# Performance work log

Hardware: AMD Instinct MI355X
Metric: run time of the kernel (lower is better)

The kernel has to match this reference:

```python
import jax, jax.numpy as jnp
import numpy as np

N = 100000
E = 1000000
IN_DIM = 128
HID = 32
HEADS = 4
OUT_DIM = 64
NEG_SLOPE = 0.2


def _gat_layer(x, src, dst, W, a_src, a_dst, b, heads, out_ch, concat):
    n = x.shape[0]
    h = (x @ W).reshape(n, heads, out_ch)                     # [N,H,C]
    s_src = jnp.sum(h * a_src, axis=-1)                        # [N,H]
    s_dst = jnp.sum(h * a_dst, axis=-1)                        # [N,H]
    e = jax.nn.leaky_relu(s_src[src] + s_dst[dst], NEG_SLOPE)  # [E,H]
    # segment softmax over incoming edges of each destination node
    m = jax.ops.segment_max(e, dst, num_segments=n)            # [N,H]
    w = jnp.exp(e - m[dst])                                    # [E,H]
    denom = jax.ops.segment_sum(w, dst, num_segments=n)        # [N,H]
    alpha = w / denom[dst]                                     # [E,H]
    out = jax.ops.segment_sum(h[src] * alpha[:, :, None], dst, num_segments=n)  # [N,H,C]
    out = out.reshape(n, heads * out_ch) if concat else out[:, 0, :]
    return out + b


def setup_inputs() -> dict:
    key = jax.random.key(0)
    ks = jax.random.split(key, 12)
    g = 0.1
    return {
        "x": jax.random.normal(ks[0], (N, IN_DIM), dtype=jnp.float32),
        "edge_index": jax.random.randint(ks[1], (2, E), 0, N, dtype=jnp.int64),
        "W1": jax.random.normal(ks[2], (IN_DIM, HEADS * HID), dtype=jnp.float32) * g,
        "a_src1": jax.random.normal(ks[3], (HEADS, HID), dtype=jnp.float32) * g,
        "a_dst1": jax.random.normal(ks[4], (HEADS, HID), dtype=jnp.float32) * g,
        "b1": jnp.zeros((HEADS * HID,), dtype=jnp.float32),
        "W2": jax.random.normal(ks[5], (HEADS * HID, OUT_DIM), dtype=jnp.float32) * g,
        "a_src2": jax.random.normal(ks[6], (1, OUT_DIM), dtype=jnp.float32) * g,
        "a_dst2": jax.random.normal(ks[7], (1, OUT_DIM), dtype=jnp.float32) * g,
        "b2": jnp.zeros((OUT_DIM,), dtype=jnp.float32),
        "fc_W": jax.random.normal(ks[8], (OUT_DIM, OUT_DIM), dtype=jnp.float32) * g,
        "fc_b": jnp.zeros((OUT_DIM,), dtype=jnp.float32),
    }


def reference(x, edge_index, W1, a_src1, a_dst1, b1, W2, a_src2, a_dst2, b2, fc_W, fc_b):
    # PyG GATConv adds self-loops by default
    loop = jnp.arange(N, dtype=edge_index.dtype)
    src = jnp.concatenate([edge_index[0], loop])
    dst = jnp.concatenate([edge_index[1], loop])
    h = _gat_layer(x, src, dst, W1, a_src1, a_dst1, b1, HEADS, HID, concat=True)
    h = jax.nn.relu(h)
    h = _gat_layer(h, src, dst, W2, a_src2, a_dst2, b2, 1, OUT_DIM, concat=False)
    h = h @ fc_W + fc_b
    return jax.nn.log_softmax(h, axis=1)
```

## Files before the change

kernel.cpp:

```cpp
#include <hip/hip_runtime.h>
#include <hip/hip_bf16.h>
#include <cfloat>

#define NN 100000
#define EE 1000000
#define TE (EE + NN)
#define C1 128
#define C2 64
#define NB1 782
#define NBKT 782
#define BCAP 4096

typedef unsigned short u16;
typedef unsigned int u32;
using bf16x8 = __attribute__((ext_vector_type(8))) short;
using f32x4  = __attribute__((ext_vector_type(4))) float;

__device__ __forceinline__ float lrelu(float v) { return v > 0.f ? v : 0.2f * v; }
__device__ __forceinline__ u16 f2bf(float f) {
    u32 b = __float_as_uint(f);
    b += 0x7fffu + ((b >> 16) & 1u);
    return (u16)(b >> 16);
}
__device__ __forceinline__ float bflo(u32 p) { return __uint_as_float(p << 16); }
__device__ __forceinline__ float bfhi(u32 p) { return __uint_as_float(p & 0xffff0000u); }

__global__ __launch_bounds__(64) void kprep(const float* __restrict__ W2,
    const float* __restrict__ as2, const float* __restrict__ ad2,
    const float* __restrict__ b2, const float* __restrict__ fcW,
    const float* __restrict__ fcb, const float* __restrict__ W1,
    u16* __restrict__ W2pbt, u16* __restrict__ W1bt,
    float* __restrict__ us, float* __restrict__ ud, float* __restrict__ b2p) {
    int b = blockIdx.x, t = threadIdx.x;
    if (b < 128) {
        float s = 0.f;
        for (int k = 0; k < 64; ++k) s = fmaf(W2[b * 64 + k], fcW[k * 64 + t], s);
        W2pbt[t * 128 + b] = f2bf(s);
    } else if (b < 130) {
        int r = (b - 128) * 64 + t;
        float s = 0.f, d = 0.f;
        for (int k = 0; k < 64; ++k) {
            float wv = W2[r * 64 + k];
            s = fmaf(wv, as2[k], s);
            d = fmaf(wv, ad2[k], d);
        }
        us[r] = s; ud[r] = d;
    } else if (b == 130) {
        float s = fcb[t];
        for (int k = 0; k < 64; ++k) s = fmaf(b2[k], fcW[k * 64 + t], s);
        b2p[t] = s;
    } else {
        int c = b - 131;
        W1bt[c * 128 + t]      = f2bf(W1[t * 128 + c]);
        W1bt[c * 128 + 64 + t] = f2bf(W1[(64 + t) * 128 + c]);
    }
}

__global__ __launch_bounds__(256) void kpassA(const int* __restrict__ esrc,
    const int* __restrict__ edst, int* __restrict__ bcnt, u32* __restrict__ bbuf) {
    int i = blockIdx.x * 256 + threadIdx.x;
    if (i >= EE / 4) return;
    int4 s4 = ((const int4*)esrc)[i];
    int4 d4 = ((const int4*)edst)[i];
    int d, s, b, pos;
    d = d4.x; s = s4.x; b = d >> 7;
    pos = atomicAdd(bcnt + b * 16, 1);
    if (pos < BCAP) bbuf[(size_t)b * BCAP + pos] = (u32)s | ((u32)(d & 127) << 17);
    d = d4.y; s = s4.y; b = d >> 7;
    pos = atomicAdd(bcnt + b * 16, 1);
    if (pos < BCAP) bbuf[(size_t)b * BCAP + pos] = (u32)s | ((u32)(d & 127) << 17);
    d = d4.z; s = s4.z; b = d >> 7;
    pos = atomicAdd(bcnt + b * 16, 1);
    if (pos < BCAP) bbuf[(size_t)b * BCAP + pos] = (u32)s | ((u32)(d & 127) << 17);
    d = d4.w; s = s4.w; b = d >> 7;
    pos = atomicAdd(bcnt + b * 16, 1);
    if (pos < BCAP) bbuf[(size_t)b * BCAP + pos] = (u32)s | ((u32)(d & 127) << 17);
}

__global__ __launch_bounds__(1024) void kbscan(const int* __restrict__ bcnt,
                                               int* __restrict__ bbase) {
    __shared__ int sm[1024];
    int t = threadIdx.x;
    int v = 0;
    if (t < NBKT) {
        int node0 = t * 128;
        int nn = NN - node0; if (nn > 128) nn = 128;
        int m = bcnt[t * 16]; if (m > BCAP) m = BCAP;
        v = m + nn;
    }
    sm[t] = v;
    __syncthreads();
    for (int off = 1; off < 1024; off <<= 1) {
        int o = 0;
        if (t >= off) o = sm[t - off];
        __syncthreads();
        if (t >= off) sm[t] += o;
        __syncthreads();
    }
    if (t < NBKT) bbase[t] = sm[t] - v;
}

__global__ __launch_bounds__(256) void kpassB(const int* __restrict__ bcnt,
    const int* __restrict__ bbase, const u32* __restrict__ bbuf,
    int* __restrict__ rowstart, int* __restrict__ eidx) {
    __shared__ int deg[128], lsc[128], cur[128];
    __shared__ int elocal[BCAP + 128];
    int b = blockIdx.x, t = threadIdx.x;
    int node0 = b * 128;
    int nNodes = NN - node0; if (nNodes > 128) nNodes = 128;
    int M = bcnt[b * 16]; if (M > BCAP) M = BCAP;
    int base = bbase[b];
    if (t < 128) deg[t] = 0;
    __syncthreads();
    const u32* bp = bbuf + (size_t)b * BCAP;
    for (int i = t; i < M; i += 256) atomicAdd(&deg[bp[i] >> 17], 1);
    __syncthreads();
    int v = 0;
    if (t < 128) { v = (t < nNodes) ? (1 + deg[t]) : 0; lsc[t] = v; }
    __syncthreads();
    for (int off = 1; off < 128; off <<= 1) {
        int o = 0;
        if (t < 128 && t >= off) o = lsc[t - off];
        __syncthreads();
        if (t < 128 && t >= off) lsc[t] += o;
        __syncthreads();
    }
    if (t < nNodes) {
        int st = lsc[t] - v;
        rowstart[node0 + t] = base + st;
        elocal[st] = node0 + t;
        cur[t] = st + 1;
    }
    if (b == NBKT - 1 && t == 0) rowstart[NN] = TE;
    __syncthreads();
    for (int i = t; i < M; i += 256) {
        u32 p = bp[i];
        int pos = atomicAdd(&cur[p >> 17], 1);
        elocal[pos] = (int)(p & 0x1FFFFu);
    }
    __syncthreads();
    int total = M + nNodes;
    for (int i = t; i < total; i += 256) eidx[base + i] = elocal[i];
}

__global__ __launch_bounds__(256, 1) void k1_mfma(const float* __restrict__ x,
    const u16* __restrict__ W1bt, const float* __restrict__ as1,
    const float* __restrict__ ad1, u16* __restrict__ h1b,
    float* __restrict__ ssrc, float* __restrict__ sdst) {
    __shared__ u16 As[128][136];
    __shared__ u16 Bs[128][136];
    int t = threadIdx.x;
    int rbase = blockIdx.x * 128;
    #pragma unroll
    for (int j = 0; j < 8; ++j) {
        int i = t + 256 * j, row = i >> 4, seg = i & 15;
        *reinterpret_cast<uint4*>(&Bs[row][seg * 8]) =
            *reinterpret_cast<const uint4*>(W1bt + row * 128 + seg * 8);
    }
    #pragma unroll
    for (int j = 0; j < 16; ++j) {
        int i = t + 256 * j, row = i >> 5, c4 = i & 31;
        int gr = rbase + row; if (gr >= NN) gr = NN - 1;
        float4 v = *reinterpret_cast<const float4*>(x + (size_t)gr * 128 + c4 * 4);
        ushort4 o2 = make_ushort4(f2bf(v.x), f2bf(v.y), f2bf(v.z), f2bf(v.w));
        *reinterpret_cast<ushort4*>(&As[row][c4 * 4]) = o2;
    }
    __syncthreads();
    int lane = t & 63, wv = t >> 6, wr = wv >> 1, wc = wv & 1;
    int fr = lane & 15, fg = lane >> 4;
    f32x4 acc[4][4];
    #pragma unroll
    for (int m = 0; m < 4; ++m)
        #pragma unroll
        for (int n = 0; n < 4; ++n) acc[m][n] = (f32x4){0.f, 0.f, 0.f, 0.f};
    #pragma unroll
    for (int kk = 0; kk < 4; ++kk) {
        bf16x8 af[4], bfr[4];
        #pragma unroll
        for (int m = 0; m < 4; ++m)
            af[m] = *reinterpret_cast<const bf16x8*>(&As[wr * 64 + m * 16 + fr][kk * 32 + fg * 8]);
        #pragma unroll
        for (int n = 0; n < 4; ++n)
            bfr[n] = *reinterpret_cast<const bf16x8*>(&Bs[wc * 64 + n * 16 + fr][kk * 32 + fg * 8]);
        #pragma unroll
        for (int m = 0; m < 4; ++m)
            #pragma unroll
            for (int n = 0; n < 4; ++n)
                acc[m][n] = __builtin_amdgcn_mfma_f32_16x16x32_bf16(af[m], bfr[n], acc[m][n], 0, 0, 0);
    }
    float asv[4], adv[4];
    #pragma unroll
    for (int n = 0; n < 4; ++n) {
        int col = wc * 64 + n * 16 + fr;
        asv[n] = as1[col]; adv[n] = ad1[col];
    }
    #pragma unroll
    for (int m = 0; m < 4; ++m)
        #pragma unroll
        for (int r = 0; r < 4; ++r) {
            int row = rbase + wr * 64 + m * 16 + fg * 4 + r;
            bool ok = row < NN;
            if (ok) {
                #pragma unroll
                for (int n = 0; n < 4; ++n)
                    h1b[(size_t)row * 128 + wc * 64 + n * 16 + fr] = f2bf(acc[m][n][r]);
            }
            float psA = acc[m][0][r] * asv[0] + acc[m][1][r] * asv[1];
            float psB = acc[m][2][r] * asv[2] + acc[m][3][r] * asv[3];
            float pdA = acc[m][0][r] * adv[0] + acc[m][1][r] * adv[1];
            float pdB = acc[m][2][r] * adv[2] + acc[m][3][r] * adv[3];
            #pragma unroll
            for (int off = 1; off <= 8; off <<= 1) {
                psA += __shfl_xor(psA, off); psB += __shfl_xor(psB, off);
                pdA += __shfl_xor(pdA, off); pdB += __shfl_xor(pdB, off);
            }
            if (fr == 0 && ok) {
                ssrc[row * 4 + 2 * wc]     = psA; sdst[row * 4 + 2 * wc]     = pdA;
                ssrc[row * 4 + 2 * wc + 1] = psB; sdst[row * 4 + 2 * wc + 1] = pdB;
            }
        }
}

__global__ __launch_bounds__(256) void agg1(const int* __restrict__ rowstart,
    const int* __restrict__ eidx, const float* __restrict__ ssrc,
    const float* __restrict__ sdst, const u16* __restrict__ h1b,
    const float* __restrict__ b1, const float* __restrict__ usv,
    const float* __restrict__ udv, u16* __restrict__ hrb,
    float* __restrict__ ssrc2, float* __restrict__ sdst2) {
    int lane = threadIdx.x & 63;
    int n = blockIdx.x * 4 + (threadIdx.x >> 6);
    if (n >= NN) return;
    int r0 = rowstart[n], deg = rowstart[n + 1] - r0;
    int h4 = lane >> 4, j16 = lane & 15;
    int half = lane >> 5, c = lane & 31, hh = c >> 3;
    float sd = sdst[n * 4 + h4];
    int s0 = (j16 < deg) ? eidx[r0 + j16] : eidx[r0];
    uint2 pv[8];
    #pragma unroll
    for (int q = 0; q < 8; ++q) {
        int s = __shfl(s0, 2 * q + half);
        pv[q] = *(const uint2*)(h1b + (size_t)s * C1 + 4 * c);
    }
    float sv0 = (j16 < deg) ? lrelu(ssrc[s0 * 4 + h4] + sd) : -FLT_MAX;
    float mx = sv0;
    #pragma unroll
    for (int off = 1; off <= 8; off <<= 1) mx = fmaxf(mx, __shfl_xor(mx, off));
    for (int base = 16; base < deg; base += 16) {
        int j = base + j16;
        float sv = (j < deg) ? lrelu(ssrc[eidx[r0 + j] * 4 + h4] + sd) : -FLT_MAX;
        #pragma unroll
        for (int off = 1; off <= 8; off <<= 1) sv = fmaxf(sv, __shfl_xor(sv, off));
        mx = fmaxf(mx, sv);
    }
    float w = (j16 < deg) ? __expf(sv0 - mx) : 0.f;
    float den = w;
    float a0 = 0.f, a1 = 0.f, a2 = 0.f, a3 = 0.f;
    #pragma unroll
    for (int q = 0; q < 8; ++q) {
        float wq = __shfl(w, (hh << 4) + 2 * q + half);
        a0 = fmaf(wq, bflo(pv[q].x), a0);
        a1 = fmaf(wq, bfhi(pv[q].x), a1);
        a2 = fmaf(wq, bflo(pv[q].y), a2);
        a3 = fmaf(wq, bfhi(pv[q].y), a3);
    }
    for (int base = 16; base < deg; base += 16) {
        int j = base + j16;
        int sreg = (j < deg) ? eidx[r0 + j] : eidx[r0];
        uint2 qv[8];
        #pragma unroll
        for (int q = 0; q < 8; ++q) {
            int s = __shfl(sreg, 2 * q + half);
            qv[q] = *(const uint2*)(h1b + (size_t)s * C1 + 4 * c);
        }
        float wb = (j < deg) ? __expf(lrelu(ssrc[sreg * 4 + h4] + sd) - mx) : 0.f;
        den += wb;
        #pragma unroll
        for (int q = 0; q < 8; ++q) {
            float wq = __shfl(wb, (hh << 4) + 2 * q + half);
            a0 = fmaf(wq, bflo(qv[q].x), a0);
            a1 = fmaf(wq, bfhi(qv[q].x), a1);
            a2 = fmaf(wq, bflo(qv[q].y), a2);
            a3 = fmaf(wq, bfhi(qv[q].y), a3);
        }
    }
    #pragma unroll
    for (int off = 1; off <= 8; off <<= 1) den += __shfl_xor(den, off);
    float dh = __shfl(den, hh << 4);
    a0 += __shfl_xor(a0, 32);
    a1 += __shfl_xor(a1, 32);
    a2 += __shfl_xor(a2, 32);
    a3 += __shfl_xor(a3, 32);
    float4 bv = *(const float4*)(b1 + 4 * c);
    float rv = 1.f / dh;
    float v0 = fmaf(a0, rv, bv.x); v0 = v0 > 0.f ? v0 : 0.f;
    float v1 = fmaf(a1, rv, bv.y); v1 = v1 > 0.f ? v1 : 0.f;
    float v2 = fmaf(a2, rv, bv.z); v2 = v2 > 0.f ? v2 : 0.f;
    float v3 = fmaf(a3, rv, bv.w); v3 = v3 > 0.f ? v3 : 0.f;
    float4 u_s = *(const float4*)(usv + 4 * c);
    float4 u_d = *(const float4*)(udv + 4 * c);
    float ps = v0 * u_s.x + v1 * u_s.y + v2 * u_s.z + v3 * u_s.w;
    float pd = v0 * u_d.x + v1 * u_d.y + v2 * u_d.z + v3 * u_d.w;
    #pragma unroll
    for (int off = 1; off <= 16; off <<= 1) {
        ps += __shfl_xor(ps, off); pd += __shfl_xor(pd, off);
    }
    if (lane == 0) { ssrc2[n] = ps; sdst2[n] = pd; }
    if (half == 0) {
        ushort4 hs = make_ushort4(f2bf(v0), f2bf(v1), f2bf(v2), f2bf(v3));
        *reinterpret_cast<ushort4*>(hrb + (size_t)n * C1 + 4 * c) = hs;
    }
}

__global__ __launch_bounds__(256, 1) void k5_mfma(const u16* __restrict__ hrb,
    const u16* __restrict__ W2pbt, u16* __restrict__ h3b) {
    __shared__ u16 As[128][136];
    __shared__ u16 Bs[64][136];
    int t = threadIdx.x;
    int rbase = blockIdx.x * 128;
    #pragma unroll
    for (int j = 0; j < 4; ++j) {
        int i = t + 256 * j, row = i >> 4, seg = i & 15;
        *reinterpret_cast<uint4*>(&Bs[row][seg * 8]) =
            *reinterpret_cast<const uint4*>(W2pbt + row * 128 + seg * 8);
    }
    #pragma unroll
    for (int j = 0; j < 8; ++j) {
        int i = t + 256 * j, row = i >> 4, seg = i & 15;
        int gr = rbase + row; if (gr >= NN) gr = NN - 1;
        *reinterpret_cast<uint4*>(&As[row][seg * 8]) =
            *reinterpret_cast<const uint4*>(hrb + (size_t)gr * 128 + seg * 8);
    }
    __syncthreads();
    int lane = t & 63, wv = t >> 6, wr = wv >> 1, wc = wv & 1;
    int fr = lane & 15, fg = lane >> 4;
    f32x4 acc[4][2];
    #pragma unroll
    for (int m = 0; m < 4; ++m)
        #pragma unroll
        for (int n = 0; n < 2; ++n) acc[m][n] = (f32x4){0.f, 0.f, 0.f, 0.f};
    #pragma unroll
    for (int kk = 0; kk < 4; ++kk) {
        bf16x8 af[4], bfr[2];
        #pragma unroll
        for (int m = 0; m < 4; ++m)
            af[m] = *reinterpret_cast<const bf16x8*>(&As[wr * 64 + m * 16 + fr][kk * 32 + fg * 8]);
        #pragma unroll
        for (int n = 0; n < 2; ++n)
            bfr[n] = *reinterpret_cast<const bf16x8*>(&Bs[wc * 32 + n * 16 + fr][kk * 32 + fg * 8]);
        #pragma unroll
        for (int m = 0; m < 4; ++m)
            #pragma unroll
            for (int n = 0; n < 2; ++n)
                acc[m][n] = __builtin_amdgcn_mfma_f32_16x16x32_bf16(af[m], bfr[n], acc[m][n], 0, 0, 0);
    }
    #pragma unroll
    for (int m = 0; m < 4; ++m)
        #pragma unroll
        for (int r = 0; r < 4; ++r) {
            int row = rbase + wr * 64 + m * 16 + fg * 4 + r;
            if (row < NN) {
                #pragma unroll
                for (int n = 0; n < 2; ++n)
                    h3b[(size_t)row * 64 + wc * 32 + n * 16 + fr] = f2bf(acc[m][n][r]);
            }
        }
}

__global__ __launch_bounds__(256) void agg2ls(const int* __restrict__ rowstart,
    const int* __restrict__ eidx, const float* __restrict__ ssrc,
    const float* __restrict__ sdst, const u16* __restrict__ h3b,
    const float* __restrict__ b2p, float* __restrict__ out) {
    int lane = threadIdx.x & 63;
    int n = blockIdx.x * 4 + (threadIdx.x >> 6);
    if (n >= NN) return;
    int r0 = rowstart[n], deg = rowstart[n + 1] - r0;
    int j16 = lane & 15, quarter = lane >> 4, c16 = lane & 15;
    float sd = sdst[n];
    int s0 = (j16 < deg) ? eidx[r0 + j16] : eidx[r0];
    uint2 pv[4];
    #pragma unroll
    for (int q = 0; q < 4; ++q) {
        int s = __shfl(s0, 4 * q + quarter);
        pv[q] = *(const uint2*)(h3b + (size_t)s * C2 + 4 * c16);
    }
    float sv0 = (j16 < deg) ? lrelu(ssrc[s0] + sd) : -FLT_MAX;
    float mx = sv0;
    #pragma unroll
    for (int off = 1; off <= 8; off <<= 1) mx = fmaxf(mx, __shfl_xor(mx, off));
    for (int base = 16; base < deg; base += 16) {
        int j = base + j16;
        float sv = (j < deg) ? lrelu(ssrc[eidx[r0 + j]] + sd) : -FLT_MAX;
        #pragma unroll
        for (int off = 1; off <= 8; off <<= 1) sv = fmaxf(sv, __shfl_xor(sv, off));
        mx = fmaxf(mx, sv);
    }
    float w = (j16 < deg) ? __expf(sv0 - mx) : 0.f;
    float den = w;
    float a0 = 0.f, a1 = 0.f, a2 = 0.f, a3 = 0.f;
    #pragma unroll
    for (int q = 0; q < 4; ++q) {
        float wq = __shfl(w, 4 * q + quarter);
        a0 = fmaf(wq, bflo(pv[q].x), a0);
        a1 = fmaf(wq, bfhi(pv[q].x), a1);
        a2 = fmaf(wq, bflo(pv[q].y), a2);
        a3 = fmaf(wq, bfhi(pv[q].y), a3);
    }
    for (int base = 16; base < deg; base += 16) {
        int j = base + j16;
        int sreg = (j < deg) ? eidx[r0 + j] : eidx[r0];
        uint2 qv[4];
        #pragma unroll
        for (int q = 0; q < 4; ++q) {
            int s = __shfl(sreg, 4 * q + quarter);
            qv[q] = *(const uint2*)(h3b + (size_t)s * C2 + 4 * c16);
        }
        float wb = (j < deg) ? __expf(lrelu(ssrc[sreg] + sd) - mx) : 0.f;
        den += wb;
        #pragma unroll
        for (int q = 0; q < 4; ++q) {
            float wq = __shfl(wb, 4 * q + quarter);
            a0 = fmaf(wq, bflo(qv[q].x), a0);
            a1 = fmaf(wq, bfhi(qv[q].x), a1);
            a2 = fmaf(wq, bflo(qv[q].y), a2);
            a3 = fmaf(wq, bfhi(qv[q].y), a3);
        }
    }
    #pragma unroll
    for (int off = 1; off <= 8; off <<= 1) den += __shfl_xor(den, off);
    a0 += __shfl_xor(a0, 16); a0 += __shfl_xor(a0, 32);
    a1 += __shfl_xor(a1, 16); a1 += __shfl_xor(a1, 32);
    a2 += __shfl_xor(a2, 16); a2 += __shfl_xor(a2, 32);
    a3 += __shfl_xor(a3, 16); a3 += __shfl_xor(a3, 32);
    float4 bv = *(const float4*)(b2p + 4 * c16);
    float rd = 1.f / den;
    float v0 = a0 * rd + bv.x, v1 = a1 * rd + bv.y;
    float v2 = a2 * rd + bv.z, v3 = a3 * rd + bv.w;
    float m4 = fmaxf(fmaxf(v0, v1), fmaxf(v2, v3));
    #pragma unroll
    for (int off = 1; off <= 8; off <<= 1) m4 = fmaxf(m4, __shfl_xor(m4, off));
    float se = __expf(v0 - m4) + __expf(v1 - m4) + __expf(v2 - m4) + __expf(v3 - m4);
    #pragma unroll
    for (int off = 1; off <= 8; off <<= 1) se += __shfl_xor(se, off);
    float lse = m4 + logf(se);
    if (quarter == 0) {
        *(float4*)(out + (size_t)n * C2 + 4 * c16) =
            make_float4(v0 - lse, v1 - lse, v2 - lse, v3 - lse);
    }
}

extern "C" void kernel_launch(void* const* d_in, const int* in_sizes, int n_in,
                              void* d_out, int out_size, void* d_ws, size_t ws_size,
                              hipStream_t stream) {
    const float* x   = (const float*)d_in[0];
    const int*   ei  = (const int*)d_in[1];
    const float* W1  = (const float*)d_in[2];
    const float* as1 = (const float*)d_in[3];
    const float* ad1 = (const float*)d_in[4];
    const float* b1  = (const float*)d_in[5];
    const float* W2  = (const float*)d_in[6];
    const float* as2 = (const float*)d_in[7];
    const float* ad2 = (const float*)d_in[8];
    const float* b2  = (const float*)d_in[9];
    const float* fcW = (const float*)d_in[10];
    const float* fcb = (const float*)d_in[11];
    float* out = (float*)d_out;

    float* ws = (float*)d_ws;
    size_t o = 0;
    u16* h1b   = (u16*)(ws + o); o += (size_t)NN * C1 / 2;
    u16* hrb   = (u16*)(ws + o); o += (size_t)NN * C1 / 2;
    float* ssrc1 = ws + o; o += (size_t)NN * 4;
    float* sdst1 = ws + o; o += (size_t)NN * 4;
    float* ssrc2 = ws + o; o += NN;
    float* sdst2 = ws + o; o += NN;
    float* usv   = ws + o; o += 128;
    float* udv   = ws + o; o += 128;
    float* b2p   = ws + o; o += 64;
    u16* W2pbt = (u16*)(ws + o); o += 64 * 128 / 2;
    u16* W1bt  = (u16*)(ws + o); o += 128 * 128 / 2;
    int* ip = (int*)(ws + o);
    int* bcnt     = ip; ip += NBKT * 16;
    int* bbase    = ip; ip += 1024;
    int* rowstart = ip; ip += NN + 2;
    int* eidx     = ip; ip += TE;
    u32* bbuf     = (u32*)ip; ip += (size_t)NBKT * BCAP;
    u16* h3b = h1b;

    const int* esrc = ei;
    const int* edst = ei + EE;

    hipMemsetAsync(bcnt, 0, (size_t)NBKT * 16 * sizeof(int), stream);

    kprep<<<259, 64, 0, stream>>>(W2, as2, ad2, b2, fcW, fcb, W1,
                                  W2pbt, W1bt, usv, udv, b2p);

    kpassA<<<(EE / 4 + 255) / 256, 256, 0, stream>>>(esrc, edst, bcnt, bbuf);
    kbscan<<<1, 1024, 0, stream>>>(bcnt, bbase);
    kpassB<<<NBKT, 256, 0, stream>>>(bcnt, bbase, bbuf, rowstart, eidx);

    k1_mfma<<<NB1, 256, 0, stream>>>(x, W1bt, as1, ad1, h1b, ssrc1, sdst1);
    agg1<<<(NN + 3) / 4, 256, 0, stream>>>(rowstart, eidx, ssrc1, sdst1, h1b, b1,
                                           usv, udv, hrb, ssrc2, sdst2);
    k5_mfma<<<NB1, 256, 0, stream>>>(hrb, W2pbt, h3b);
    agg2ls<<<(NN + 3) / 4, 256, 0, stream>>>(rowstart, eidx, ssrc2, sdst2, h3b, b2p, out);
}
```

Before: 216.2 us.

## Fuse CSR build into layer-1 aggregation and merge prep into bucketing kernel

Merges the weight-prep kernel into the edge-bucketing kernel as extra blocks, and folds the per-bucket CSR construction (kpassB) into agg1. agg1 now builds each bucket's local edge list in shared memory and aggregates its 128 nodes straight from LDS, with 4 waves looping over nodes. It still writes rowstart/eidx for layer 2. The aim is fewer launches and no global round trip for eidx in layer 1. The cost is that agg1 drops from 25000 small blocks to 782 large ones with about 17KB of LDS each, which lowers parallelism and occupancy, and each bucket's aggregation is serialized behind its CSR build. Also hoists the ssrc loads earlier in agg2.

```diff
diff --git a/kernel.cpp b/kernel.cpp
--- a/kernel.cpp
+++ b/kernel.cpp
@@ -10,6 +10,7 @@
 #define NB1 782
 #define NBKT 782
 #define BCAP 4096
+#define NPA 977
 
 typedef unsigned short u16;
 typedef unsigned int u32;
@@ -25,13 +26,36 @@
 __device__ __forceinline__ float bflo(u32 p) { return __uint_as_float(p << 16); }
 __device__ __forceinline__ float bfhi(u32 p) { return __uint_as_float(p & 0xffff0000u); }
 
-__global__ __launch_bounds__(64) void kprep(const float* __restrict__ W2,
-    const float* __restrict__ as2, const float* __restrict__ ad2,
-    const float* __restrict__ b2, const float* __restrict__ fcW,
-    const float* __restrict__ fcb, const float* __restrict__ W1,
-    u16* __restrict__ W2pbt, u16* __restrict__ W1bt,
+__global__ __launch_bounds__(256) void kpassA(const int* __restrict__ esrc,
+    const int* __restrict__ edst, int* __restrict__ bcnt, u32* __restrict__ bbuf,
+    const float* __restrict__ W2, const float* __restrict__ as2,
+    const float* __restrict__ ad2, const float* __restrict__ b2,
+    const float* __restrict__ fcW, const float* __restrict__ fcb,
+    const float* __restrict__ W1, u16* __restrict__ W2pbt, u16* __restrict__ W1bt,
     float* __restrict__ us, float* __restrict__ ud, float* __restrict__ b2p) {
-    int b = blockIdx.x, t = threadIdx.x;
+    int blk = blockIdx.x;
+    if (blk < NPA) {
+        int i = blk * 256 + threadIdx.x;
+        if (i >= EE / 4) return;
+        int4 s4 = ((const int4*)esrc)[i];
+        int4 d4 = ((const int4*)edst)[i];
+        int d, s, b, pos;
+        d = d4.x; s = s4.x; b = d >> 7;
+        pos = atomicAdd(bcnt + b * 16, 1);
+        if (pos < BCAP) bbuf[(size_t)b * BCAP + pos] = (u32)s | ((u32)(d & 127) << 17);
+        d = d4.y; s = s4.y; b = d >> 7;
+        pos = atomicAdd(bcnt + b * 16, 1);
+        if (pos < BCAP) bbuf[(size_t)b * BCAP + pos] = (u32)s | ((u32)(d & 127) << 17);
+        d = d4.z; s = s4.z; b = d >> 7;
+        pos = atomicAdd(bcnt + b * 16, 1);
+        if (pos < BCAP) bbuf[(size_t)b * BCAP + pos] = (u32)s | ((u32)(d & 127) << 17);
+        d = d4.w; s = s4.w; b = d >> 7;
+        pos = atomicAdd(bcnt + b * 16, 1);
+        if (pos < BCAP) bbuf[(size_t)b * BCAP + pos] = (u32)s | ((u32)(d & 127) << 17);
+        return;
+    }
+    int b = blk - NPA, t = threadIdx.x;
+    if (t >= 64) return;
     if (b < 128) {
         float s = 0.f;
         for (int k = 0; k < 64; ++k) s = fmaf(W2[b * 64 + k], fcW[k * 64 + t], s);
@@ -56,27 +80,6 @@
     }
 }
 
-__global__ __launch_bounds__(256) void kpassA(const int* __restrict__ esrc,
-    const int* __restrict__ edst, int* __restrict__ bcnt, u32* __restrict__ bbuf) {
-    int i = blockIdx.x * 256 + threadIdx.x;
-    if (i >= EE / 4) return;
-    int4 s4 = ((const int4*)esrc)[i];
-    int4 d4 = ((const int4*)edst)[i];
-    int d, s, b, pos;
-    d = d4.x; s = s4.x; b = d >> 7;
-    pos = atomicAdd(bcnt + b * 16, 1);
-    if (pos < BCAP) bbuf[(size_t)b * BCAP + pos] = (u32)s | ((u32)(d & 127) << 17);
-    d = d4.y; s = s4.y; b = d >> 7;
-    pos = atomicAdd(bcnt + b * 16, 1);
-    if (pos < BCAP) bbuf[(size_t)b * BCAP + pos] = (u32)s | ((u32)(d & 127) << 17);
-    d = d4.z; s = s4.z; b = d >> 7;
-    pos = atomicAdd(bcnt + b * 16, 1);
-    if (pos < BCAP) bbuf[(size_t)b * BCAP + pos] = (u32)s | ((u32)(d & 127) << 17);
-    d = d4.w; s = s4.w; b = d >> 7;
-    pos = atomicAdd(bcnt + b * 16, 1);
-    if (pos < BCAP) bbuf[(size_t)b * BCAP + pos] = (u32)s | ((u32)(d & 127) << 17);
-}
-
 __global__ __launch_bounds__(1024) void kbscan(const int* __restrict__ bcnt,
                                                int* __restrict__ bbase) {
     __shared__ int sm[1024];
@@ -98,49 +101,6 @@
         __syncthreads();
     }
     if (t < NBKT) bbase[t] = sm[t] - v;
-}
-
-__global__ __launch_bounds__(256) void kpassB(const int* __restrict__ bcnt,
-    const int* __restrict__ bbase, const u32* __restrict__ bbuf,
-    int* __restrict__ rowstart, int* __restrict__ eidx) {
-    __shared__ int deg[128], lsc[128], cur[128];
-    __shared__ int elocal[BCAP + 128];
-    int b = blockIdx.x, t = threadIdx.x;
-    int node0 = b * 128;
-    int nNodes = NN - node0; if (nNodes > 128) nNodes = 128;
-    int M = bcnt[b * 16]; if (M > BCAP) M = BCAP;
-    int base = bbase[b];
-    if (t < 128) deg[t] = 0;
-    __syncthreads();
-    const u32* bp = bbuf + (size_t)b * BCAP;
-    for (int i = t; i < M; i += 256) atomicAdd(&deg[bp[i] >> 17], 1);
-    __syncthreads();
-    int v = 0;
-    if (t < 128) { v = (t < nNodes) ? (1 + deg[t]) : 0; lsc[t] = v; }
-    __syncthreads();
-    for (int off = 1; off < 128; off <<= 1) {
-        int o = 0;
-        if (t < 128 && t >= off) o = lsc[t - off];
-        __syncthreads();
-        if (t < 128 && t >= off) lsc[t] += o;
-        __syncthreads();
-    }
-    if (t < nNodes) {
-        int st = lsc[t] - v;
-        rowstart[node0 + t] = base + st;
-        elocal[st] = node0 + t;
-        cur[t] = st + 1;
-    }
-    if (b == NBKT - 1 && t == 0) rowstart[NN] = TE;
-    __syncthreads();
-    for (int i = t; i < M; i += 256) {
-        u32 p = bp[i];
-        int pos = atomicAdd(&cur[p >> 17], 1);
-        elocal[pos] = (int)(p & 0x1FFFFu);
-    }
-    __syncthreads();
-    int total = M + nNodes;
-    for (int i = t; i < total; i += 256) eidx[base + i] = elocal[i];
 }
 
 __global__ __launch_bounds__(256, 1) void k1_mfma(const float* __restrict__ x,
@@ -221,93 +181,139 @@
         }
 }
 
-__global__ __launch_bounds__(256) void agg1(const int* __restrict__ rowstart,
-    const int* __restrict__ eidx, const float* __restrict__ ssrc,
-    const float* __restrict__ sdst, const u16* __restrict__ h1b,
-    const float* __restrict__ b1, const float* __restrict__ usv,
-    const float* __restrict__ udv, u16* __restrict__ hrb,
-    float* __restrict__ ssrc2, float* __restrict__ sdst2) {
-    int lane = threadIdx.x & 63;
-    int n = blockIdx.x * 4 + (threadIdx.x >> 6);
-    if (n >= NN) return;
-    int r0 = rowstart[n], deg = rowstart[n + 1] - r0;
+__global__ __launch_bounds__(256) void agg1(const int* __restrict__ bcnt,
+    const int* __restrict__ bbase, const u32* __restrict__ bbuf,
+    const float* __restrict__ ssrc, const float* __restrict__ sdst,
+    const u16* __restrict__ h1b, const float* __restrict__ b1,
+    const float* __restrict__ usv, const float* __restrict__ udv,
+    u16* __restrict__ hrb, float* __restrict__ ssrc2, float* __restrict__ sdst2,
+    int* __restrict__ rowstart, int* __restrict__ eidx) {
+    __shared__ int deg[128], lsc[128], cur[128];
+    __shared__ int elocal[BCAP + 128];
+    int b = blockIdx.x, t = threadIdx.x;
+    int node0 = b * 128;
+    int nNodes = NN - node0; if (nNodes > 128) nNodes = 128;
+    int M = bcnt[b * 16]; if (M > BCAP) M = BCAP;
+    int base = bbase[b];
+    if (t < 128) deg[t] = 0;
+    __syncthreads();
+    const u32* bp = bbuf + (size_t)b * BCAP;
+    for (int i = t; i < M; i += 256) atomicAdd(&deg[bp[i] >> 17], 1);
+    __syncthreads();
+    int v = 0;
+    if (t < 128) { v = (t < nNodes) ? (1 + deg[t]) : 0; lsc[t] = v; }
+    __syncthreads();
+    for (int off = 1; off < 128; off <<= 1) {
+        int o = 0;
+        if (t < 128 && t >= off) o = lsc[t - off];
+        __syncthreads();
+        if (t < 128 && t >= off) lsc[t] += o;
+        __syncthreads();
+    }
+    if (t < nNodes) {
+        int st = lsc[t] - v;
+        rowstart[node0 + t] = base + st;
+        elocal[st] = node0 + t;
+        cur[t] = st + 1;
+    }
+    if (b == NBKT - 1 && t == 0) rowstart[NN] = TE;
+    __syncthreads();
+    for (int i = t; i < M; i += 256) {
+        u32 p = bp[i];
+        int pos = atomicAdd(&cur[p >> 17], 1);
+        elocal[pos] = (int)(p & 0x1FFFFu);
+    }
+    __syncthreads();
+    int total = M + nNodes;
+    for (int i = t; i < total; i += 256) eidx[base + i] = elocal[i];
+    __syncthreads();
+
+    int lane = t & 63, wid = t >> 6;
     int h4 = lane >> 4, j16 = lane & 15;
     int half = lane >> 5, c = lane & 31, hh = c >> 3;
-    float sd = sdst[n * 4 + h4];
-    int s0 = (j16 < deg) ? eidx[r0 + j16] : eidx[r0];
-    uint2 pv[8];
-    #pragma unroll
-    for (int q = 0; q < 8; ++q) {
-        int s = __shfl(s0, 2 * q + half);
-        pv[q] = *(const uint2*)(h1b + (size_t)s * C1 + 4 * c);
-    }
-    float sv0 = (j16 < deg) ? lrelu(ssrc[s0 * 4 + h4] + sd) : -FLT_MAX;
-    float mx = sv0;
-    #pragma unroll
-    for (int off = 1; off <= 8; off <<= 1) mx = fmaxf(mx, __shfl_xor(mx, off));
-    for (int base = 16; base < deg; base += 16) {
-        int j = base + j16;
-        float sv = (j < deg) ? lrelu(ssrc[eidx[r0 + j] * 4 + h4] + sd) : -FLT_MAX;
-        #pragma unroll
-        for (int off = 1; off <= 8; off <<= 1) sv = fmaxf(sv, __shfl_xor(sv, off));
-        mx = fmaxf(mx, sv);
-    }
-    float w = (j16 < deg) ? __expf(sv0 - mx) : 0.f;
-    float den = w;
-    float a0 = 0.f, a1 = 0.f, a2 = 0.f, a3 = 0.f;
-    #pragma unroll
-    for (int q = 0; q < 8; ++q) {
-        float wq = __shfl(w, (hh << 4) + 2 * q + half);
-        a0 = fmaf(wq, bflo(pv[q].x), a0);
-        a1 = fmaf(wq, bfhi(pv[q].x), a1);
-        a2 = fmaf(wq, bflo(pv[q].y), a2);
-        a3 = fmaf(wq, bfhi(pv[q].y), a3);
-    }
-    for (int base = 16; base < deg; base += 16) {
-        int j = base + j16;
-        int sreg = (j < deg) ? eidx[r0 + j] : eidx[r0];
-        uint2 qv[8];
-        #pragma unroll
-        for (int q = 0; q < 8; ++q) {
-            int s = __shfl(sreg, 2 * q + half);
-            qv[q] = *(const uint2*)(h1b + (size_t)s * C1 + 4 * c);
-        }
-        float wb = (j < deg) ? __expf(lrelu(ssrc[sreg * 4 + h4] + sd) - mx) : 0.f;
-        den += wb;
-        #pragma unroll
-        for (int q = 0; q < 8; ++q) {
-            float wq = __shfl(wb, (hh << 4) + 2 * q + half);
-            a0 = fmaf(wq, bflo(qv[q].x), a0);
-            a1 = fmaf(wq, bfhi(qv[q].x), a1);
-            a2 = fmaf(wq, bflo(qv[q].y), a2);
-            a3 = fmaf(wq, bfhi(qv[q].y), a3);
-        }
-    }
-    #pragma unroll
-    for (int off = 1; off <= 8; off <<= 1) den += __shfl_xor(den, off);
-    float dh = __shfl(den, hh << 4);
-    a0 += __shfl_xor(a0, 32);
-    a1 += __shfl_xor(a1, 32);
-    a2 += __shfl_xor(a2, 32);
-    a3 += __shfl_xor(a3, 32);
-    float4 bv = *(const float4*)(b1 + 4 * c);
-    float rv = 1.f / dh;
-    float v0 = fmaf(a0, rv, bv.x); v0 = v0 > 0.f ? v0 : 0.f;
-    float v1 = fmaf(a1, rv, bv.y); v1 = v1 > 0.f ? v1 : 0.f;
-    float v2 = fmaf(a2, rv, bv.z); v2 = v2 > 0.f ? v2 : 0.f;
-    float v3 = fmaf(a3, rv, bv.w); v3 = v3 > 0.f ? v3 : 0.f;
+    float4 bv  = *(const float4*)(b1 + 4 * c);
     float4 u_s = *(const float4*)(usv + 4 * c);
     float4 u_d = *(const float4*)(udv + 4 * c);
-    float ps = v0 * u_s.x + v1 * u_s.y + v2 * u_s.z + v3 * u_s.w;
-    float pd = v0 * u_d.x + v1 * u_d.y + v2 * u_d.z + v3 * u_d.w;
-    #pragma unroll
-    for (int off = 1; off <= 16; off <<= 1) {
-        ps += __shfl_xor(ps, off); pd += __shfl_xor(pd, off);
-    }
-    if (lane == 0) { ssrc2[n] = ps; sdst2[n] = pd; }
-    if (half == 0) {
-        ushort4 hs = make_ushort4(f2bf(v0), f2bf(v1), f2bf(v2), f2bf(v3));
-        *reinterpret_cast<ushort4*>(hrb + (size_t)n * C1 + 4 * c) = hs;
+    for (int i = wid; i < nNodes; i += 4) {
+        int n = node0 + i;
+        int dgi = deg[i] + 1;
+        int st  = lsc[i] - dgi;
+        float sd = sdst[n * 4 + h4];
+        int s0 = elocal[st + ((j16 < dgi) ? j16 : 0)];
+        float sraw = ssrc[s0 * 4 + h4];
+        uint2 pv[8];
+        #pragma unroll
+        for (int q = 0; q < 8; ++q) {
+            int s = __shfl(s0, 2 * q + half);
+            pv[q] = *(const uint2*)(h1b + (size_t)s * C1 + 4 * c);
+        }
+        float sv0 = (j16 < dgi) ? lrelu(sraw + sd) : -FLT_MAX;
+        float mx = sv0;
+        #pragma unroll
+        for (int off = 1; off <= 8; off <<= 1) mx = fmaxf(mx, __shfl_xor(mx, off));
+        for (int bb = 16; bb < dgi; bb += 16) {
+            int j = bb + j16;
+            float sv = -FLT_MAX;
+            if (j < dgi) sv = lrelu(ssrc[elocal[st + j] * 4 + h4] + sd);
+            #pragma unroll
+            for (int off = 1; off <= 8; off <<= 1) sv = fmaxf(sv, __shfl_xor(sv, off));
+            mx = fmaxf(mx, sv);
+        }
+        float w = (j16 < dgi) ? __expf(sv0 - mx) : 0.f;
+        float den = w;
+        float a0 = 0.f, a1 = 0.f, a2 = 0.f, a3 = 0.f;
+        #pragma unroll
+        for (int q = 0; q < 8; ++q) {
+            float wq = __shfl(w, (hh << 4) + 2 * q + half);
+            a0 = fmaf(wq, bflo(pv[q].x), a0);
+            a1 = fmaf(wq, bfhi(pv[q].x), a1);
+            a2 = fmaf(wq, bflo(pv[q].y), a2);
+            a3 = fmaf(wq, bfhi(pv[q].y), a3);
+        }
+        for (int bb = 16; bb < dgi; bb += 16) {
+            int j = bb + j16;
+            int sreg = elocal[st + ((j < dgi) ? j : 0)];
+            float wsr = ssrc[sreg * 4 + h4];
+            uint2 qv[8];
+            #pragma unroll
+            for (int q = 0; q < 8; ++q) {
+                int s = __shfl(sreg, 2 * q + half);
+                qv[q] = *(const uint2*)(h1b + (size_t)s * C1 + 4 * c);
+            }
+            float wb = (j < dgi) ? __expf(lrelu(wsr + sd) - mx) : 0.f;
+            den += wb;
+            #pragma unroll
+            for (int q = 0; q < 8; ++q) {
+                float wq = __shfl(wb, (hh << 4) + 2 * q + half);
+                a0 = fmaf(wq, bflo(qv[q].x), a0);
+                a1 = fmaf(wq, bfhi(qv[q].x), a1);
+                a2 = fmaf(wq, bflo(qv[q].y), a2);
+                a3 = fmaf(wq, bfhi(qv[q].y), a3);
+            }
+        }
+        #pragma unroll
+        for (int off = 1; off <= 8; off <<= 1) den += __shfl_xor(den, off);
+        float dh = __shfl(den, hh << 4);
+        a0 += __shfl_xor(a0, 32);
+        a1 += __shfl_xor(a1, 32);
+        a2 += __shfl_xor(a2, 32);
+        a3 += __shfl_xor(a3, 32);
+        float rv = 1.f / dh;
+        float v0 = fmaf(a0, rv, bv.x); v0 = v0 > 0.f ? v0 : 0.f;
+        float v1 = fmaf(a1, rv, bv.y); v1 = v1 > 0.f ? v1 : 0.f;
+        float v2 = fmaf(a2, rv, bv.z); v2 = v2 > 0.f ? v2 : 0.f;
+        float v3 = fmaf(a3, rv, bv.w); v3 = v3 > 0.f ? v3 : 0.f;
+        float ps = v0 * u_s.x + v1 * u_s.y + v2 * u_s.z + v3 * u_s.w;
+        float pd = v0 * u_d.x + v1 * u_d.y + v2 * u_d.z + v3 * u_d.w;
+        #pragma unroll
+        for (int off = 1; off <= 16; off <<= 1) {
+            ps += __shfl_xor(ps, off); pd += __shfl_xor(pd, off);
+        }
+        if (lane == 0) { ssrc2[n] = ps; sdst2[n] = pd; }
+        if (half == 0) {
+            ushort4 hs = make_ushort4(f2bf(v0), f2bf(v1), f2bf(v2), f2bf(v3));
+            *reinterpret_cast<ushort4*>(hrb + (size_t)n * C1 + 4 * c) = hs;
+        }
     }
 }
 
@@ -377,19 +383,21 @@
     int j16 = lane & 15, quarter = lane >> 4, c16 = lane & 15;
     float sd = sdst[n];
     int s0 = (j16 < deg) ? eidx[r0 + j16] : eidx[r0];
+    float sraw = ssrc[s0];
     uint2 pv[4];
     #pragma unroll
     for (int q = 0; q < 4; ++q) {
         int s = __shfl(s0, 4 * q + quarter);
         pv[q] = *(const uint2*)(h3b + (size_t)s * C2 + 4 * c16);
     }
-    float sv0 = (j16 < deg) ? lrelu(ssrc[s0] + sd) : -FLT_MAX;
+    float sv0 = (j16 < deg) ? lrelu(sraw + sd) : -FLT_MAX;
     float mx = sv0;
     #pragma unroll
     for (int off = 1; off <= 8; off <<= 1) mx = fmaxf(mx, __shfl_xor(mx, off));
     for (int base = 16; base < deg; base += 16) {
         int j = base + j16;
-        float sv = (j < deg) ? lrelu(ssrc[eidx[r0 + j]] + sd) : -FLT_MAX;
+        float sv = -FLT_MAX;
+        if (j < deg) sv = lrelu(ssrc[eidx[r0 + j]] + sd);
         #pragma unroll
         for (int off = 1; off <= 8; off <<= 1) sv = fmaxf(sv, __shfl_xor(sv, off));
         mx = fmaxf(mx, sv);
@@ -408,13 +416,14 @@
     for (int base = 16; base < deg; base += 16) {
         int j = base + j16;
         int sreg = (j < deg) ? eidx[r0 + j] : eidx[r0];
+        float wsr = ssrc[sreg];
         uint2 qv[4];
         #pragma unroll
         for (int q = 0; q < 4; ++q) {
             int s = __shfl(sreg, 4 * q + quarter);
             qv[q] = *(const uint2*)(h3b + (size_t)s * C2 + 4 * c16);
         }
-        float wb = (j < deg) ? __expf(lrelu(ssrc[sreg] + sd) - mx) : 0.f;
+        float wb = (j < deg) ? __expf(lrelu(wsr + sd) - mx) : 0.f;
         den += wb;
         #pragma unroll
         for (int q = 0; q < 4; ++q) {
@@ -491,16 +500,14 @@
 
     hipMemsetAsync(bcnt, 0, (size_t)NBKT * 16 * sizeof(int), stream);
 
-    kprep<<<259, 64, 0, stream>>>(W2, as2, ad2, b2, fcW, fcb, W1,
-                                  W2pbt, W1bt, usv, udv, b2p);
-
-    kpassA<<<(EE / 4 + 255) / 256, 256, 0, stream>>>(esrc, edst, bcnt, bbuf);
+    kpassA<<<NPA + 259, 256, 0, stream>>>(esrc, edst, bcnt, bbuf,
+                                          W2, as2, ad2, b2, fcW, fcb, W1,
+                                          W2pbt, W1bt, usv, udv, b2p);
     kbscan<<<1, 1024, 0, stream>>>(bcnt, bbase);
-    kpassB<<<NBKT, 256, 0, stream>>>(bcnt, bbase, bbuf, rowstart, eidx);
 
     k1_mfma<<<NB1, 256, 0, stream>>>(x, W1bt, as1, ad1, h1b, ssrc1, sdst1);
-    agg1<<<(NN + 3) / 4, 256, 0, stream>>>(rowstart, eidx, ssrc1, sdst1, h1b, b1,
-                                           usv, udv, hrb, ssrc2, sdst2);
+    agg1<<<NBKT, 256, 0, stream>>>(bcnt, bbase, bbuf, ssrc1, sdst1, h1b, b1,
+                                   usv, udv, hrb, ssrc2, sdst2, rowstart, eidx);
     k5_mfma<<<NB1, 256, 0, stream>>>(hrb, W2pbt, h3b);
     agg2ls<<<(NN + 3) / 4, 256, 0, stream>>>(rowstart, eidx, ssrc2, sdst2, h3b, b2p, out);
 }
```

After: 216.1 us. About the same (-0.1%).
